# Kernel optimization log

Measured on AMD Instinct MI355X. Metric: run time of the kernel, lower is better.

Reference implementation:

```python
import jax, jax.numpy as jnp
import numpy as np

B, F, T, D, O = 8192, 512, 64, 6, 128
N_INTERNAL = 2 ** D - 1  # 63
N_LEAVES = 2 ** D        # 64


def smooth_step(t):
    tc = jnp.clip(t, -0.5, 0.5)
    return -2.0 * tc ** 3 + 1.5 * tc + 0.5


def setup_inputs() -> dict:
    key = jax.random.key(0)
    k1, k2, k3, k4 = jax.random.split(key, 4)
    x = jax.random.normal(k1, (B, F), dtype=jnp.float32)
    # Stacked per-node Linear weights in BFS (heap) order: node i -> row i.
    W_nodes = jax.random.normal(k2, (N_INTERNAL, F, T), dtype=jnp.float32) * (1.0 / np.sqrt(F))
    b_nodes = jax.random.normal(k3, (N_INTERNAL, T), dtype=jnp.float32) * 0.01
    # Per-leaf mixing weight [out_features, num_trees], leaves in BFS order.
    W_leaf = jax.random.normal(k4, (N_LEAVES, O, T), dtype=jnp.float32)
    return {"x": x, "W_nodes": W_nodes, "b_nodes": b_nodes, "W_leaf": W_leaf}


def reference(x, W_nodes, b_nodes, W_leaf):
    n_internal = W_nodes.shape[0]
    depth = int(np.log2(n_internal + 1))
    # All internal-node gates in one stacked GEMM: [B, n_internal, T]
    s = smooth_step(jnp.einsum('bf,nft->bnt', x, W_nodes) + b_nodes[None, :, :])
    b, _, t = s.shape
    prob = jnp.ones((b, 1, t), dtype=s.dtype)  # root prob
    start = 0
    for lvl in range(depth):
        width = 2 ** lvl
        s_l = s[:, start:start + width]  # [B, width, T], nodes at this level
        start += width
        # node local j -> children local 2j (left, prob*s) and 2j+1 (right, prob*(1-s))
        prob = jnp.stack([prob * s_l, prob * (1.0 - s_l)], axis=2).reshape(b, 2 * width, t)
    # prob: [B, n_leaves, T]; mix per-leaf, per-tree weights -> [B, O]
    out = jnp.einsum('blt,lot->bo', prob, W_leaf)
    return out
```

## Files before the change

kernel.cpp:

```cpp
#include <hip/hip_runtime.h>
#include <hip/hip_fp16.h>

#define BATCH 8192
#define FDIM  512
#define NTREE 64
#define NODES 63
#define ODIM  128
#define NJP   4096
#define K2    4096
#define TPG   8

typedef _Float16 f16;
typedef _Float16 f16x2 __attribute__((ext_vector_type(2)));
typedef _Float16 f16x4 __attribute__((ext_vector_type(4)));
typedef _Float16 f16x8 __attribute__((ext_vector_type(8)));
typedef float    f32x4 __attribute__((ext_vector_type(4)));

#define XH_OFF   0
#define XH_SZ    ((size_t)BATCH*FDIM*2)
#define WNH_OFF  (XH_OFF + XH_SZ)
#define WNH_SZ   ((size_t)NJP*FDIM*2)
#define WLT_OFF  (WNH_OFF + WNH_SZ)
#define WLT_SZ   ((size_t)ODIM*K2*2)
#define PS_OFF   (WLT_OFF + WLT_SZ)
#define PS_SZ    ((size_t)TPG*BATCH*ODIM*4)
#define WS_NEEDED (PS_OFF + PS_SZ)

__device__ __forceinline__ float smooth_step_f(float t) {
    float tc = fminf(fmaxf(t, -0.5f), 0.5f);
    return fmaf(tc, fmaf(-2.0f * tc, tc, 1.5f), 0.5f);
}

__device__ __forceinline__ int sw_off(int row, int g) {
    return ((row >> 3) * 512) + (((row & 7) * 8 + (g ^ (row & 7))) * 8);
}

__global__ __launch_bounds__(256)
void prep_kernel(const float* __restrict__ x, const float* __restrict__ wn,
                 const float* __restrict__ wl,
                 f16* __restrict__ xf, f16* __restrict__ wnf, f16* __restrict__ wlf)
{
    const int bid = blockIdx.x, tid = threadIdx.x;
    if (bid < 512) {
        const int bx = bid >> 3, k0 = bid & 7;
        f16* dst = xf + ((size_t)bx * 8192 + (size_t)k0 * 1024) * 8;
        #pragma unroll
        for (int c = 0; c < 4; ++c) {
            int fid  = c * 256 + tid;
            int lane = fid & 63, ks = (fid >> 6) & 1, rg = (fid >> 7) & 7;
            int row  = bx * 128 + rg * 16 + (lane & 15);
            int k    = k0 * 64 + (ks * 4 + (lane >> 4)) * 8;
            const float* s = x + (size_t)row * FDIM + k;
            float4 a = *(const float4*)s, b = *(const float4*)(s + 4);
            f16x8 v = { (f16)a.x, (f16)a.y, (f16)a.z, (f16)a.w,
                        (f16)b.x, (f16)b.y, (f16)b.z, (f16)b.w };
            *(f16x8*)(dst + (size_t)fid * 8) = v;
        }
    } else if (bid < 768) {
        const int id = bid - 512;
        const int t0 = (id >> 4) * 4;
        const int n  = tid & 63;
        const int k8 = (id & 15) * 4 + (tid >> 6);
        float4 q[8];
        if (n != NODES) {
            #pragma unroll
            for (int e = 0; e < 8; ++e)
                q[e] = *(const float4*)(wn + ((size_t)n * FDIM + k8 * 8 + e) * NTREE + t0);
        }
        #pragma unroll
        for (int j = 0; j < 4; ++j) {
            int t  = t0 + j;
            int tp = t >> 1;
            int cg = (t & 1) * 4 + (n >> 4);
            size_t chunk = (size_t)tp * 8192 + (size_t)(k8 >> 3) * 1024 + cg * 128
                         + ((k8 >> 2) & 1) * 64 + (k8 & 3) * 16 + (n & 15);
            f16x8 v;
            if (n == NODES) {
                #pragma unroll
                for (int e = 0; e < 8; ++e) v[e] = (f16)0.0f;
            } else {
                const float* qf = (const float*)q;
                #pragma unroll
                for (int e = 0; e < 8; ++e) v[e] = (f16)qf[e * 4 + j];
            }
            *(f16x8*)(wnf + chunk * 8) = v;
        }
    } else {
        const int id = bid - 768;
        const int t0 = (id >> 2) * 4;
        const int o  = tid & 127;
        const int l8 = (id & 3) * 2 + (tid >> 7);
        float4 q[8];
        #pragma unroll
        for (int e = 0; e < 8; ++e)
            q[e] = *(const float4*)(wl + ((size_t)(l8 * 8 + e) * ODIM + o) * NTREE + t0);
        #pragma unroll
        for (int j = 0; j < 4; ++j) {
            int t  = t0 + j;
            int tp = t >> 1, h = t & 1;
            size_t chunk = (size_t)tp * 2048 + (size_t)h * 1024 + (o >> 4) * 128
                         + (l8 >> 2) * 64 + (l8 & 3) * 16 + (o & 15);
            const float* qf = (const float*)q;
            f16x8 v;
            #pragma unroll
            for (int e = 0; e < 8; ++e) v[e] = (f16)qf[e * 4 + j];
            *(f16x8*)(wlf + chunk * 8) = v;
        }
    }
}

__global__ __launch_bounds__(256, 4)
void fused_tree(const f16* __restrict__ xhF, const f16* __restrict__ wnhF,
                const float* __restrict__ bn, const f16* __restrict__ wltF,
                float* __restrict__ partial)
{
    __shared__ __align__(16) f16 SH[16512];
    const int tid  = threadIdx.x;
    const int lane = tid & 63;
    const int w    = tid >> 6;
    const int wm   = w & 1;
    const int wq   = w >> 1;
    const int tpg  = blockIdx.y;

    const int frow = tid & 63;
    const int ftr  = (tid >> 6) & 1;
    const int sub  = tid >> 7;

    const f16x8* __restrict__ xv = (const f16x8*)xhF;
    const f16x8* __restrict__ wv = (const f16x8*)wnhF;
    const f16x8* __restrict__ lv = (const f16x8*)wltF;
    const size_t xb = (size_t)(blockIdx.x >> 1) * 8192
                    + (size_t)((blockIdx.x & 1) * 4 + wm * 2) * 128 + lane;

    f32x4 lacc[2][4] = {};

    for (int tpi = 0; tpi < 4; ++tpi) {
        const int tp = tpg * 4 + tpi;
        const int j0 = tp * 128;

        const size_t wb = (size_t)tp * 8192 + (size_t)wq * 512 + lane;
        f32x4 acc[2][4] = {};
        #pragma unroll 2
        for (int k0 = 0; k0 < 8; ++k0) {
            #pragma unroll
            for (int ks = 0; ks < 2; ++ks) {
                f16x8 bfr[4];
                #pragma unroll
                for (int tn = 0; tn < 4; ++tn)
                    bfr[tn] = wv[wb + k0 * 1024 + tn * 128 + ks * 64];
                #pragma unroll
                for (int tm = 0; tm < 2; ++tm) {
                    f16x8 afr = xv[xb + k0 * 1024 + tm * 128 + ks * 64];
                    #pragma unroll
                    for (int tn = 0; tn < 4; ++tn)
                        acc[tm][tn] = __builtin_amdgcn_mfma_f32_16x16x32_f16(afr, bfr[tn], acc[tm][tn], 0, 0, 0);
                }
            }
        }

        #pragma unroll
        for (int tn = 0; tn < 4; ++tn) {
            int col = wq * 64 + tn * 16 + (lane & 15);
            int nn  = col & 63;
            int tt  = (j0 + col) >> 6;
            float bias = (nn < NODES) ? bn[nn * NTREE + tt] : 0.0f;
            #pragma unroll
            for (int tm = 0; tm < 2; ++tm) {
                #pragma unroll
                for (int r = 0; r < 4; ++r) {
                    int row = wm * 32 + tm * 16 + (lane >> 4) * 4 + r;
                    SH[row * 130 + col] = (f16)smooth_step_f(acc[tm][tn][r] + bias);
                }
            }
        }
        __syncthreads();

        {
            const f16* gp = &SH[frow * 130 + ftr * 64];
            float pq[16];
            {
                float g0 = (float)gp[0];
                float p  = sub ? 1.0f - g0 : g0;
                float s1 = (float)gp[1 + sub];
                pq[0] = p * s1; pq[1] = p * (1.0f - s1);
                #pragma unroll
                for (int m = 1; m >= 0; --m) {
                    float s = (float)gp[3 + sub * 2 + m]; float pp = pq[m];
                    pq[2 * m] = pp * s; pq[2 * m + 1] = pp * (1.0f - s);
                }
                #pragma unroll
                for (int m = 3; m >= 0; --m) {
                    float s = (float)gp[7 + sub * 4 + m]; float pp = pq[m];
                    pq[2 * m] = pp * s; pq[2 * m + 1] = pp * (1.0f - s);
                }
                #pragma unroll
                for (int m = 7; m >= 0; --m) {
                    float s = (float)gp[15 + sub * 8 + m]; float pp = pq[m];
                    pq[2 * m] = pp * s; pq[2 * m + 1] = pp * (1.0f - s);
                }
            }
            f16x8 ov[4];
            #pragma unroll
            for (int ii = 0; ii < 16; ++ii) {
                float s5 = (float)gp[31 + sub * 16 + ii];
                float p  = pq[ii];
                int ll   = 2 * ii;
                ov[ll >> 3][ll & 7]       = (f16)(p * s5);
                ov[ll >> 3][(ll & 7) + 1] = (f16)(p * (1.0f - s5));
            }
            #pragma unroll
            for (int q = 0; q < 4; ++q)
                *(f16x8*)&SH[8320 + ftr * 4096 + sw_off(frow, sub * 4 + q)] = ov[q];
        }
        __syncthreads();

        const size_t lb = (size_t)tp * 2048 + (size_t)wq * 512 + lane;
        #pragma unroll
        for (int h = 0; h < 2; ++h) {
            #pragma unroll
            for (int ks = 0; ks < 2; ++ks) {
                int g = ks * 4 + (lane >> 4);
                f16x8 bfr[4];
                #pragma unroll
                for (int tn = 0; tn < 4; ++tn)
                    bfr[tn] = lv[lb + h * 1024 + tn * 128 + ks * 64];
                #pragma unroll
                for (int tm = 0; tm < 2; ++tm) {
                    int m = wm * 32 + tm * 16 + (lane & 15);
                    f16x8 afr = *(const f16x8*)&SH[8320 + h * 4096 + sw_off(m, g)];
                    #pragma unroll
                    for (int tn = 0; tn < 4; ++tn)
                        lacc[tm][tn] = __builtin_amdgcn_mfma_f32_16x16x32_f16(afr, bfr[tn], lacc[tm][tn], 0, 0, 0);
                }
            }
        }
        __syncthreads();
    }

    float* dst = partial + (size_t)tpg * BATCH * ODIM;
    const int row0 = blockIdx.x * 64;
    #pragma unroll
    for (int tn = 0; tn < 4; ++tn) {
        int o = wq * 64 + tn * 16 + (lane & 15);
        #pragma unroll
        for (int tm = 0; tm < 2; ++tm) {
            #pragma unroll
            for (int r = 0; r < 4; ++r) {
                int row = row0 + wm * 32 + tm * 16 + (lane >> 4) * 4 + r;
                dst[(size_t)row * ODIM + o] = lacc[tm][tn][r];
            }
        }
    }
}

__global__ void reduce_kernel(const float* __restrict__ partial, float* __restrict__ out) {
    size_t i = ((size_t)blockIdx.x * blockDim.x + threadIdx.x) * 4;
    f32x4 a = *(const f32x4*)(partial + i);
    #pragma unroll
    for (int k = 1; k < TPG; ++k)
        a += *(const f32x4*)(partial + (size_t)k * BATCH * ODIM + i);
    *(f32x4*)(out + i) = a;
}

#define ROWS 8
__global__ __launch_bounds__(256, 2)
void soft_tree_fallback(const float* __restrict__ x, const float* __restrict__ Wn,
                        const float* __restrict__ bn, const float* __restrict__ Wl,
                        float* __restrict__ out)
{
    __shared__ __half s_lds[ROWS][NODES][NTREE];
    const int lane = threadIdx.x & 63;
    const int w    = threadIdx.x >> 6;
    const long row0 = (long)blockIdx.x * ROWS;
    for (int n = w; n < NODES; n += 4) {
        const float* wp = Wn + ((long)n * FDIM) * NTREE + lane;
        const float* xp = x + row0 * FDIM;
        float acc[ROWS];
        #pragma unroll
        for (int r = 0; r < ROWS; ++r) acc[r] = 0.0f;
        #pragma unroll 8
        for (int f = 0; f < FDIM; ++f) {
            float wv = wp[(long)f * NTREE];
            #pragma unroll
            for (int r = 0; r < ROWS; ++r)
                acc[r] = fmaf(xp[r * FDIM + f], wv, acc[r]);
        }
        float bias = bn[n * NTREE + lane];
        #pragma unroll
        for (int r = 0; r < ROWS; ++r)
            s_lds[r][n][lane] = __float2half(smooth_step_f(acc[r] + bias));
    }
    __syncthreads();
    const int r0 = w * 2, r1 = w * 2 + 1;
    float pr0[64], pr1[64];
    {
        pr0[0] = 1.0f; pr1[0] = 1.0f;
        int base = 0;
        #pragma unroll
        for (int lvl = 0; lvl < 6; ++lvl) {
            const int width = 1 << lvl;
            #pragma unroll
            for (int i = width - 1; i >= 0; --i) {
                float sa = __half2float(s_lds[r0][base + i][lane]);
                float sb = __half2float(s_lds[r1][base + i][lane]);
                float pa = pr0[i], pb = pr1[i];
                pr0[2 * i] = pa * sa; pr0[2 * i + 1] = pa * (1.0f - sa);
                pr1[2 * i] = pb * sb; pr1[2 * i + 1] = pb * (1.0f - sb);
            }
            base += width;
        }
    }
    for (int o = 0; o < ODIM; ++o) {
        const float* wlp = Wl + (long)o * NTREE + lane;
        float c0 = 0.0f, c1 = 0.0f;
        #pragma unroll
        for (int l = 0; l < 64; ++l) {
            float wv = wlp[(long)l * (ODIM * NTREE)];
            c0 = fmaf(pr0[l], wv, c0);
            c1 = fmaf(pr1[l], wv, c1);
        }
        #pragma unroll
        for (int off = 32; off > 0; off >>= 1) {
            c0 += __shfl_xor(c0, off, 64);
            c1 += __shfl_xor(c1, off, 64);
        }
        if (lane == 0) {
            out[(row0 + r0) * ODIM + o] = c0;
            out[(row0 + r1) * ODIM + o] = c1;
        }
    }
}

extern "C" void kernel_launch(void* const* d_in, const int* in_sizes, int n_in,
                              void* d_out, int out_size, void* d_ws, size_t ws_size,
                              hipStream_t stream) {
    const float* x  = (const float*)d_in[0];
    const float* Wn = (const float*)d_in[1];
    const float* bn = (const float*)d_in[2];
    const float* Wl = (const float*)d_in[3];
    float* out = (float*)d_out;

    if (ws_size < WS_NEEDED) {
        soft_tree_fallback<<<BATCH / ROWS, 256, 0, stream>>>(x, Wn, bn, Wl, out);
        return;
    }

    f16*   xh  = (f16*)((char*)d_ws + XH_OFF);
    f16*   wnh = (f16*)((char*)d_ws + WNH_OFF);
    f16*   wlt = (f16*)((char*)d_ws + WLT_OFF);
    float* ps  = (float*)((char*)d_ws + PS_OFF);

    prep_kernel<<<832, 256, 0, stream>>>(x, Wn, Wl, xh, wnh, wlt);
    fused_tree<<<dim3(BATCH / 64, TPG), 256, 0, stream>>>(xh, wnh, bn, wlt, ps);
    reduce_kernel<<<(BATCH * ODIM) / (256 * 4), 256, 0, stream>>>(ps, out);
}
```

Before: 154.0 us.

## Keep tree probability computation in registers via node permutation and lane shuffles

Permutes the gate-weight columns and biases (rho mapping) so that the MFMA output layout directly matches the tree traversal. Probabilities are then computed in registers with wave shuffles, and the resulting fragments feed the leaf GEMM as A operands, which removes the shared-memory staging and all block barriers. Each block now handles 128 rows with one wave per 32 rows. Launch bounds drop to 2 waves per SIMD to leave room for the larger register accumulators. The trade-off is much higher register pressure and lower occupancy, plus a more intricate index mapping that is easy to get wrong.

```diff
diff --git a/kernel.cpp b/kernel.cpp
--- a/kernel.cpp
+++ b/kernel.cpp
@@ -22,7 +22,9 @@
 #define WNH_SZ   ((size_t)NJP*FDIM*2)
 #define WLT_OFF  (WNH_OFF + WNH_SZ)
 #define WLT_SZ   ((size_t)ODIM*K2*2)
-#define PS_OFF   (WLT_OFF + WLT_SZ)
+#define BNF_OFF  (WLT_OFF + WLT_SZ)
+#define BNF_SZ   ((size_t)NTREE*64*4)
+#define PS_OFF   (BNF_OFF + BNF_SZ)
 #define PS_SZ    ((size_t)TPG*BATCH*ODIM*4)
 #define WS_NEEDED (PS_OFF + PS_SZ)
 
@@ -31,16 +33,30 @@
     return fmaf(tc, fmaf(-2.0f * tc, tc, 1.5f), 0.5f);
 }
 
-__device__ __forceinline__ int sw_off(int row, int g) {
-    return ((row >> 3) * 512) + (((row & 7) * 8 + (g ^ (row & 7))) * 8);
+__device__ __forceinline__ int rho(int n) {
+    if (n < 15)  return n;
+    if (n == 63) return 15;
+    if (n < 31) { int m = n - 15; int hi = (m >= 8) ? 1 : 0; int mm = m - hi * 8;
+                  return 16 + (mm >> 1) * 4 + (mm & 1) + hi * 2; }
+    return n + 1;
 }
 
 __global__ __launch_bounds__(256)
 void prep_kernel(const float* __restrict__ x, const float* __restrict__ wn,
-                 const float* __restrict__ wl,
-                 f16* __restrict__ xf, f16* __restrict__ wnf, f16* __restrict__ wlf)
+                 const float* __restrict__ wl, const float* __restrict__ bn,
+                 f16* __restrict__ xf, f16* __restrict__ wnf, f16* __restrict__ wlf,
+                 float* __restrict__ bnf)
 {
     const int bid = blockIdx.x, tid = threadIdx.x;
+    if (bid == 832) {
+        #pragma unroll
+        for (int i = 0; i < 16; ++i) {
+            int idx = tid * 16 + i;
+            int n = idx & 63, t = idx >> 6;
+            bnf[t * 64 + rho(n)] = (n < NODES) ? bn[n * NTREE + t] : 0.0f;
+        }
+        return;
+    }
     if (bid < 512) {
         const int bx = bid >> 3, k0 = bid & 7;
         f16* dst = xf + ((size_t)bx * 8192 + (size_t)k0 * 1024) * 8;
@@ -61,6 +77,7 @@
         const int t0 = (id >> 4) * 4;
         const int n  = tid & 63;
         const int k8 = (id & 15) * 4 + (tid >> 6);
+        const int rr = rho(n);
         float4 q[8];
         if (n != NODES) {
             #pragma unroll
@@ -71,9 +88,9 @@
         for (int j = 0; j < 4; ++j) {
             int t  = t0 + j;
             int tp = t >> 1;
-            int cg = (t & 1) * 4 + (n >> 4);
+            int cg = (t & 1) * 4 + (rr >> 4);
             size_t chunk = (size_t)tp * 8192 + (size_t)(k8 >> 3) * 1024 + cg * 128
-                         + ((k8 >> 2) & 1) * 64 + (k8 & 3) * 16 + (n & 15);
+                         + ((k8 >> 2) & 1) * 64 + (k8 & 3) * 16 + (rr & 15);
             f16x8 v;
             if (n == NODES) {
                 #pragma unroll
@@ -109,145 +126,130 @@
     }
 }
 
-__global__ __launch_bounds__(256, 4)
+__global__ __launch_bounds__(256, 2)
 void fused_tree(const f16* __restrict__ xhF, const f16* __restrict__ wnhF,
-                const float* __restrict__ bn, const f16* __restrict__ wltF,
+                const float* __restrict__ bnF, const f16* __restrict__ wltF,
                 float* __restrict__ partial)
 {
-    __shared__ __align__(16) f16 SH[16512];
     const int tid  = threadIdx.x;
     const int lane = tid & 63;
     const int w    = tid >> 6;
-    const int wm   = w & 1;
-    const int wq   = w >> 1;
+    const int q    = lane >> 4;
+    const int c    = lane & 15;
     const int tpg  = blockIdx.y;
-
-    const int frow = tid & 63;
-    const int ftr  = (tid >> 6) & 1;
-    const int sub  = tid >> 7;
 
     const f16x8* __restrict__ xv = (const f16x8*)xhF;
     const f16x8* __restrict__ wv = (const f16x8*)wnhF;
     const f16x8* __restrict__ lv = (const f16x8*)wltF;
-    const size_t xb = (size_t)(blockIdx.x >> 1) * 8192
-                    + (size_t)((blockIdx.x & 1) * 4 + wm * 2) * 128 + lane;
-
-    f32x4 lacc[2][4] = {};
+    const size_t xb = (size_t)blockIdx.x * 8192 + (size_t)(w * 2) * 128 + lane;
+
+    f32x4 lacc[2][8] = {};
 
     for (int tpi = 0; tpi < 4; ++tpi) {
         const int tp = tpg * 4 + tpi;
-        const int j0 = tp * 128;
-
-        const size_t wb = (size_t)tp * 8192 + (size_t)wq * 512 + lane;
-        f32x4 acc[2][4] = {};
+
+        const size_t wb = (size_t)tp * 8192 + lane;
+        f32x4 acc[8][2] = {};
         #pragma unroll 2
         for (int k0 = 0; k0 < 8; ++k0) {
             #pragma unroll
             for (int ks = 0; ks < 2; ++ks) {
-                f16x8 bfr[4];
-                #pragma unroll
-                for (int tn = 0; tn < 4; ++tn)
-                    bfr[tn] = wv[wb + k0 * 1024 + tn * 128 + ks * 64];
-                #pragma unroll
-                for (int tm = 0; tm < 2; ++tm) {
-                    f16x8 afr = xv[xb + k0 * 1024 + tm * 128 + ks * 64];
-                    #pragma unroll
-                    for (int tn = 0; tn < 4; ++tn)
-                        acc[tm][tn] = __builtin_amdgcn_mfma_f32_16x16x32_f16(afr, bfr[tn], acc[tm][tn], 0, 0, 0);
+                f16x8 xf0 = xv[xb + k0 * 1024 + 0 * 128 + ks * 64];
+                f16x8 xf1 = xv[xb + k0 * 1024 + 1 * 128 + ks * 64];
+                #pragma unroll
+                for (int tn = 0; tn < 8; ++tn) {
+                    f16x8 afr = wv[wb + k0 * 1024 + tn * 128 + ks * 64];
+                    acc[tn][0] = __builtin_amdgcn_mfma_f32_16x16x32_f16(afr, xf0, acc[tn][0], 0, 0, 0);
+                    acc[tn][1] = __builtin_amdgcn_mfma_f32_16x16x32_f16(afr, xf1, acc[tn][1], 0, 0, 0);
                 }
             }
         }
 
         #pragma unroll
-        for (int tn = 0; tn < 4; ++tn) {
-            int col = wq * 64 + tn * 16 + (lane & 15);
-            int nn  = col & 63;
-            int tt  = (j0 + col) >> 6;
-            float bias = (nn < NODES) ? bn[nn * NTREE + tt] : 0.0f;
-            #pragma unroll
-            for (int tm = 0; tm < 2; ++tm) {
-                #pragma unroll
-                for (int r = 0; r < 4; ++r) {
-                    int row = wm * 32 + tm * 16 + (lane >> 4) * 4 + r;
-                    SH[row * 130 + col] = (f16)smooth_step_f(acc[tm][tn][r] + bias);
+        for (int tn = 0; tn < 8; ++tn) {
+            int tree = tp * 2 + (tn >> 2);
+            f32x4 bv = *(const f32x4*)(bnF + tree * 64 + (tn & 3) * 16 + q * 4);
+            #pragma unroll
+            for (int tb = 0; tb < 2; ++tb)
+                #pragma unroll
+                for (int r = 0; r < 4; ++r)
+                    acc[tn][tb][r] = smooth_step_f(acc[tn][tb][r] + bv[r]);
+        }
+
+        f16x8 pf[2][2][2];
+        #pragma unroll
+        for (int wt = 0; wt < 2; ++wt) {
+            #pragma unroll
+            for (int tb = 0; tb < 2; ++tb) {
+                const f32x4 s0 = acc[wt * 4 + 0][tb];
+                const f32x4 s1 = acc[wt * 4 + 1][tb];
+                const f32x4 s2 = acc[wt * 4 + 2][tb];
+                const f32x4 s3 = acc[wt * 4 + 3][tb];
+                float t0  = __shfl(s0[0], c);
+                float t1  = __shfl(s0[1], c);
+                float t2  = __shfl(s0[2], c);
+                float t3  = __shfl(s0[3], c);
+                float t4  = __shfl(s0[0], c + 16);
+                float t5  = __shfl(s0[1], c + 16);
+                float t6  = __shfl(s0[2], c + 16);
+                float t7  = __shfl(s0[3], c + 16);
+                float t8  = __shfl(s0[0], c + 32);
+                float t9  = __shfl(s0[1], c + 32);
+                float t10 = __shfl(s0[2], c + 32);
+                float t11 = __shfl(s0[3], c + 32);
+                float t12 = __shfl(s0[0], c + 48);
+                float t13 = __shfl(s0[1], c + 48);
+                float t14 = __shfl(s0[2], c + 48);
+                float P1 = t0,        P2 = 1.0f - t0;
+                float P3 = P1 * t1,   P4 = P1 - P3, P5 = P2 * t2,  P6 = P2 - P5;
+                float P7 = P3 * t3,   P8 = P3 - P7, P9 = P4 * t4,  P10 = P4 - P9;
+                float P11 = P5 * t5,  P12 = P5 - P11, P13 = P6 * t6, P14 = P6 - P13;
+                int qa = q & 1, qb = q & 2;
+                float PA  = qb ? (qa ? P10 : P9 ) : (qa ? P8  : P7 );
+                float sga = qb ? (qa ? t10 : t9 ) : (qa ? t8  : t7 );
+                float PB  = qb ? (qa ? P14 : P13) : (qa ? P12 : P11);
+                float sgb = qb ? (qa ? t14 : t13) : (qa ? t12 : t11);
+                float E0 = PA * sga, E1 = PA - E0, E2 = PB * sgb, E3 = PB - E2;
+                float F0 = E0 * s1[0], F1 = E0 - F0, F2 = E1 * s1[1], F3 = E1 - F2;
+                float G0 = E2 * s1[2], G1 = E2 - G0, G2 = E3 * s1[3], G3 = E3 - G2;
+                float L0 = F0 * s2[0], L1 = F0 - L0, L2 = F1 * s2[1], L3 = F1 - L2;
+                float L4 = F2 * s2[2], L5 = F2 - L4, L6 = F3 * s2[3], L7 = F3 - L6;
+                float M0 = G0 * s3[0], M1 = G0 - M0, M2 = G1 * s3[1], M3 = G1 - M2;
+                float M4 = G2 * s3[2], M5 = G2 - M4, M6 = G3 * s3[3], M7 = G3 - M6;
+                f16x8 pa = { (f16)L0, (f16)L1, (f16)L2, (f16)L3,
+                             (f16)L4, (f16)L5, (f16)L6, (f16)L7 };
+                f16x8 pb = { (f16)M0, (f16)M1, (f16)M2, (f16)M3,
+                             (f16)M4, (f16)M5, (f16)M6, (f16)M7 };
+                pf[wt][tb][0] = pa;
+                pf[wt][tb][1] = pb;
+            }
+        }
+
+        const size_t lb = (size_t)tp * 2048 + lane;
+        #pragma unroll
+        for (int wt = 0; wt < 2; ++wt) {
+            #pragma unroll
+            for (int ks = 0; ks < 2; ++ks) {
+                #pragma unroll
+                for (int to = 0; to < 8; ++to) {
+                    f16x8 blf = lv[lb + wt * 1024 + to * 128 + ks * 64];
+                    lacc[0][to] = __builtin_amdgcn_mfma_f32_16x16x32_f16(pf[wt][0][ks], blf, lacc[0][to], 0, 0, 0);
+                    lacc[1][to] = __builtin_amdgcn_mfma_f32_16x16x32_f16(pf[wt][1][ks], blf, lacc[1][to], 0, 0, 0);
                 }
             }
         }
-        __syncthreads();
-
-        {
-            const f16* gp = &SH[frow * 130 + ftr * 64];
-            float pq[16];
-            {
-                float g0 = (float)gp[0];
-                float p  = sub ? 1.0f - g0 : g0;
-                float s1 = (float)gp[1 + sub];
-                pq[0] = p * s1; pq[1] = p * (1.0f - s1);
-                #pragma unroll
-                for (int m = 1; m >= 0; --m) {
-                    float s = (float)gp[3 + sub * 2 + m]; float pp = pq[m];
-                    pq[2 * m] = pp * s; pq[2 * m + 1] = pp * (1.0f - s);
-                }
-                #pragma unroll
-                for (int m = 3; m >= 0; --m) {
-                    float s = (float)gp[7 + sub * 4 + m]; float pp = pq[m];
-                    pq[2 * m] = pp * s; pq[2 * m + 1] = pp * (1.0f - s);
-                }
-                #pragma unroll
-                for (int m = 7; m >= 0; --m) {
-                    float s = (float)gp[15 + sub * 8 + m]; float pp = pq[m];
-                    pq[2 * m] = pp * s; pq[2 * m + 1] = pp * (1.0f - s);
-                }
-            }
-            f16x8 ov[4];
-            #pragma unroll
-            for (int ii = 0; ii < 16; ++ii) {
-                float s5 = (float)gp[31 + sub * 16 + ii];
-                float p  = pq[ii];
-                int ll   = 2 * ii;
-                ov[ll >> 3][ll & 7]       = (f16)(p * s5);
-                ov[ll >> 3][(ll & 7) + 1] = (f16)(p * (1.0f - s5));
-            }
-            #pragma unroll
-            for (int q = 0; q < 4; ++q)
-                *(f16x8*)&SH[8320 + ftr * 4096 + sw_off(frow, sub * 4 + q)] = ov[q];
-        }
-        __syncthreads();
-
-        const size_t lb = (size_t)tp * 2048 + (size_t)wq * 512 + lane;
-        #pragma unroll
-        for (int h = 0; h < 2; ++h) {
-            #pragma unroll
-            for (int ks = 0; ks < 2; ++ks) {
-                int g = ks * 4 + (lane >> 4);
-                f16x8 bfr[4];
-                #pragma unroll
-                for (int tn = 0; tn < 4; ++tn)
-                    bfr[tn] = lv[lb + h * 1024 + tn * 128 + ks * 64];
-                #pragma unroll
-                for (int tm = 0; tm < 2; ++tm) {
-                    int m = wm * 32 + tm * 16 + (lane & 15);
-                    f16x8 afr = *(const f16x8*)&SH[8320 + h * 4096 + sw_off(m, g)];
-                    #pragma unroll
-                    for (int tn = 0; tn < 4; ++tn)
-                        lacc[tm][tn] = __builtin_amdgcn_mfma_f32_16x16x32_f16(afr, bfr[tn], lacc[tm][tn], 0, 0, 0);
-                }
-            }
-        }
-        __syncthreads();
     }
 
     float* dst = partial + (size_t)tpg * BATCH * ODIM;
-    const int row0 = blockIdx.x * 64;
+    const int row0 = blockIdx.x * 128 + w * 32;
     #pragma unroll
-    for (int tn = 0; tn < 4; ++tn) {
-        int o = wq * 64 + tn * 16 + (lane & 15);
-        #pragma unroll
-        for (int tm = 0; tm < 2; ++tm) {
+    for (int tb = 0; tb < 2; ++tb) {
+        #pragma unroll
+        for (int to = 0; to < 8; ++to) {
             #pragma unroll
             for (int r = 0; r < 4; ++r) {
-                int row = row0 + wm * 32 + tm * 16 + (lane >> 4) * 4 + r;
-                dst[(size_t)row * ODIM + o] = lacc[tm][tn][r];
+                int row = row0 + tb * 16 + q * 4 + r;
+                dst[(size_t)row * ODIM + to * 16 + c] = lacc[tb][to][r];
             }
         }
     }
@@ -348,9 +350,10 @@
     f16*   xh  = (f16*)((char*)d_ws + XH_OFF);
     f16*   wnh = (f16*)((char*)d_ws + WNH_OFF);
     f16*   wlt = (f16*)((char*)d_ws + WLT_OFF);
+    float* bnf = (float*)((char*)d_ws + BNF_OFF);
     float* ps  = (float*)((char*)d_ws + PS_OFF);
 
-    prep_kernel<<<832, 256, 0, stream>>>(x, Wn, Wl, xh, wnh, wlt);
-    fused_tree<<<dim3(BATCH / 64, TPG), 256, 0, stream>>>(xh, wnh, bn, wlt, ps);
+    prep_kernel<<<833, 256, 0, stream>>>(x, Wn, Wl, bn, xh, wnh, wlt, bnf);
+    fused_tree<<<dim3(BATCH / 128, TPG), 256, 0, stream>>>(xh, wnh, bnf, wlt, ps);
     reduce_kernel<<<(BATCH * ODIM) / (256 * 4), 256, 0, stream>>>(ps, out);
 }
```

New measurement: 166.6 us. 8.2% more time.
